# Kernel tuning notes

Measured on AMD Instinct MI355X. Metric: run time of the kernel, lower is better.

## Reference

```python
import jax, jax.numpy as jnp
import numpy as np

B, A, F, D, C = 256, 128, 512, 6, 512  # batch, max_atoms, atom_features, max_degree, conv_width


def setup_inputs() -> dict:
    key = jax.random.key(0)
    k1, k2, k3, k4 = jax.random.split(key, 4)
    atoms = jax.random.normal(k1, (B, A, F), dtype=jnp.float32)
    # neighbour indices in [0, A); pad entries beyond each atom's degree with -1
    neigh = jax.random.randint(k2, (B, A, D), 0, A)
    deg = jax.random.randint(k3, (B, A, 1), 0, D)  # degrees in 0..D-1
    bonds = jnp.where(jnp.arange(D)[None, None, :] < deg, neigh, -1)
    # one Dense(conv_width) per degree: stacked kernels [D, F, C] and biases [D, C]
    W = jax.random.normal(k4, (D, F, C), dtype=jnp.float32) * 0.02
    b = jnp.zeros((D, C), dtype=jnp.float32)
    return {"atoms": atoms, "bonds": bonds, "W": W, "b": b}


def reference(atoms, bonds, W, b):
    d_max = bonds.shape[-1]
    # per-atom degree = count of non -1 neighbour slots  [B, A, 1]
    degrees = jnp.sum(bonds != -1, axis=-1, keepdims=True)
    # shift lookup by 1 so that padded (-1) neighbours index a zero row
    padded = jnp.pad(atoms, ((0, 0), (1, 1), (0, 0)))  # [B, A+2, F]
    idx = bonds + 1  # [B, A, D]
    # per-sample gather of neighbour features -> [B, A, D, F]
    neigh_feats = jax.vmap(lambda ref, i: ref[i])(padded, idx)
    summed = jnp.sum(neigh_feats, axis=2) + atoms  # [B, A, F]
    # apply all degree-specific dense layers, then mask-select by degree
    dense = jnp.einsum('baf,dfc->badc', summed, W) + b  # [B, A, D, C]
    masks = (degrees[..., None] == jnp.arange(d_max).reshape(1, 1, d_max, 1)).astype(dense.dtype)
    return jnp.sum(dense * masks, axis=2)  # [B, A, C]
```

## Files before the change

### kernel.cpp

```cpp
#include <hip/hip_runtime.h>
#include <hip/hip_bf16.h>


#define NB 256
#define NA 128
#define NF 512
#define ND 6
#define NC 512
#define NATOMS (NB * NA)

#define NT_TRANS 1536
#define NT_BUCK  32

typedef __attribute__((ext_vector_type(8))) short frag8;
typedef __attribute__((ext_vector_type(4))) float f32x4;
typedef __attribute__((ext_vector_type(4))) unsigned int u32x4;

static __device__ inline unsigned short f2bu(float f) {
    __hip_bfloat16 h = __float2bfloat16(f);
    return *reinterpret_cast<unsigned short*>(&h);
}
static __device__ inline unsigned int pack2(float a, float b) {
    return (unsigned int)f2bu(a) | ((unsigned int)f2bu(b) << 16);
}
static __device__ inline float b2f(unsigned short u) {
    __hip_bfloat16 h;
    *reinterpret_cast<unsigned short*>(&h) = u;
    return __bfloat162float(h);
}
static __device__ inline void async16(const void* g, void* l) {
    __builtin_amdgcn_global_load_lds(
        (const __attribute__((address_space(1))) void*)g,
        (__attribute__((address_space(3))) void*)l, 16, 0, 0);
}

__global__ __launch_bounds__(256) void prep_misc(
    const float* __restrict__ W, __hip_bfloat16* __restrict__ Wt,
    const int* __restrict__ bonds, int* __restrict__ counts,
    int* __restrict__ bucket) {
    const int bid = blockIdx.x;
    const int tid = threadIdx.x;
    __shared__ float t[32][33];
    __shared__ int lcnt[ND];
    __shared__ int lbase[ND];

    if (bid < NT_TRANS) {
        const int tx = tid & 31, ty = tid >> 5;
        const int c0 = (bid & 15) * 32;
        const int f0 = ((bid >> 4) & 15) * 32;
        const int d  = bid >> 8;
        #pragma unroll
        for (int r = 0; r < 32; r += 8)
            t[ty + r][tx] =
                W[((size_t)(d * NF + f0 + ty + r)) * NC + c0 + tx];
        __syncthreads();
        #pragma unroll
        for (int r = 0; r < 32; r += 8)
            Wt[((size_t)(d * NC + c0 + ty + r)) * NF + f0 + tx] =
                __float2bfloat16(t[tx][ty + r]);
        return;
    }
    const int b = bid - NT_TRANS;
    if (tid < ND) lcnt[tid] = 0;
    __syncthreads();
    int deg[4], loc[4], gg[4];
    #pragma unroll
    for (int i = 0; i < 4; ++i) {
        int g = b * 1024 + i * 256 + tid;
        gg[i] = g;
        int dg = 0;
        #pragma unroll
        for (int j = 0; j < ND; ++j) dg += (bonds[g * ND + j] >= 0);
        deg[i] = dg;
        loc[i] = atomicAdd(&lcnt[dg], 1);
    }
    __syncthreads();
    if (tid < ND) lbase[tid] = atomicAdd(&counts[tid], lcnt[tid]);
    __syncthreads();
    #pragma unroll
    for (int i = 0; i < 4; ++i)
        bucket[deg[i] * NATOMS + lbase[deg[i]] + loc[i]] = gg[i];
}

__global__ __launch_bounds__(512, 2) void sum_mol(
    const float* __restrict__ atoms, const int* __restrict__ bonds,
    __hip_bfloat16* __restrict__ summed) {
    __shared__ __align__(16) __hip_bfloat16 mol[NA * NF];
    char* molB = (char*)mol;
    const int m   = blockIdx.x;
    const int tid = threadIdx.x;

    const float4* a4 = (const float4*)atoms + (size_t)m * (NA * NF / 4);
    #pragma unroll 4
    for (int i = 0; i < 32; ++i) {
        float4 v = a4[i * 512 + tid];
        const int r  = i * 4 + (tid >> 7);
        const int co = tid & 127;
        uint2 pk; pk.x = pack2(v.x, v.y); pk.y = pack2(v.z, v.w);
        *(uint2*)(molB + r * 1024 + (((co >> 1) ^ (r & 7)) << 4) + (co & 1) * 8) = pk;
    }
    __syncthreads();

    const int a  = tid >> 2;
    const int qd = tid & 3;
    const int* bd = bonds + (size_t)(m * NA + a) * ND;
    int   nb[ND], x7[ND];
    float msk[ND];
    #pragma unroll
    for (int j = 0; j < ND; ++j) {
        int n = bd[j];
        msk[j] = (n >= 0) ? 1.0f : 0.0f;
        nb[j]  = (n >= 0) ? n : 0;
        x7[j]  = nb[j] & 7;
    }
    const int a7 = a & 7;

    u32x4 psum[16];
    #pragma unroll
    for (int ci = 0; ci < 16; ++ci) {
        const int c = qd * 16 + ci;
        const frag8 s = *(const frag8*)(molB + a * 1024 + ((c ^ a7) << 4));
        float acc[8];
        #pragma unroll
        for (int e = 0; e < 8; ++e) acc[e] = b2f((unsigned short)s[e]);
        #pragma unroll
        for (int j = 0; j < ND; ++j) {
            const frag8 v = *(const frag8*)(molB + nb[j] * 1024 + ((c ^ x7[j]) << 4));
            #pragma unroll
            for (int e = 0; e < 8; ++e)
                acc[e] = fmaf(b2f((unsigned short)v[e]), msk[j], acc[e]);
        }
        u32x4 o;
        o[0] = pack2(acc[0], acc[1]); o[1] = pack2(acc[2], acc[3]);
        o[2] = pack2(acc[4], acc[5]); o[3] = pack2(acc[6], acc[7]);
        psum[ci] = o;
    }

    __syncthreads();
    #pragma unroll
    for (int ci = 0; ci < 16; ++ci) {
        const int c = qd * 16 + ci;
        *(u32x4*)(molB + a * 1024 + ((c ^ a7) << 4)) = psum[ci];
    }
    __syncthreads();

    const int chunk = tid & 63;
    char* dst = (char*)summed + (size_t)m * (NA * NF * 2);
    #pragma unroll
    for (int t = 0; t < 16; ++t) {
        const int row = t * 8 + (tid >> 6);
        u32x4 v = *(const u32x4*)(molB + row * 1024 + ((chunk ^ (row & 7)) << 4));
        *(u32x4*)(dst + row * 1024 + chunk * 16) = v;
    }
}

__global__ __launch_bounds__(512, 4) void gemm_deg(
    const __hip_bfloat16* __restrict__ summed, const __hip_bfloat16* __restrict__ Wt,
    const float* __restrict__ bias, const int* __restrict__ counts,
    const int* __restrict__ bucket, float* __restrict__ out) {
    const int L  = blockIdx.x + 24 * blockIdx.y;
    const int q  = L >> 3;
    const int p  = ((q >> 1) << 3) + (L & 7);
    const int d  = p % ND;
    const int m0 = (p / ND) * 128;
    const int n0 = (q & 1) * 256;
    const int Md = counts[d];
    if (m0 >= Md) return;

    __shared__ __align__(16) char smem[74240];
    char* const sAb   = smem;
    char* const sBb   = smem + 24576;
    int*  const sRows = (int*)(smem + 73728);

    const int tid = threadIdx.x;
    if (tid < 128) {
        int r = m0 + tid;
        sRows[tid] = (r < Md) ? bucket[d * NATOMS + r] : -1;
    }
    __syncthreads();

    const int lane = tid & 63;
    const int w    = tid >> 6;

    const int sr = lane >> 2;
    const int sl = lane & 3;
    const int gseg = sl ^ ((sr >> 1) & 3);

    const char* smB = (const char*)summed;
    const char* wtB = (const char*)Wt + (size_t)(d * NC + n0) * 1024;
    int g0 = sRows[w * 16 + sr];
    const size_t gA0 = (size_t)((g0 < 0) ? 0 : g0) * 1024;
    const size_t gB0 = (size_t)(w * 16 + sr) * 1024;
    const size_t gB1 = (size_t)(128 + w * 16 + sr) * 1024;

    const int quad = lane >> 4, l16 = lane & 15;
    const int xr2  = (l16 >> 1) & 3;
    const int wy = w >> 2, wx = w & 3;

    f32x4 acc[4][4];
    #pragma unroll
    for (int i = 0; i < 4; ++i)
        #pragma unroll
        for (int j = 0; j < 4; ++j) acc[i][j] = (f32x4)0.0f;

    auto stage = [&](int buf, int kt) {
        const int koff = kt * 64 + gseg * 16;
        async16(smB + gA0 + koff, sAb + buf * 8192 + w * 1024);
        async16(wtB + gB0 + koff, sBb + buf * 16384 + w * 1024);
        async16(wtB + gB1 + koff, sBb + buf * 16384 + 8192 + w * 1024);
    };
    auto compute = [&](int buf) {
        const __hip_bfloat16* A  = (const __hip_bfloat16*)(sAb + buf * 8192);
        const __hip_bfloat16* Bm = (const __hip_bfloat16*)(sBb + buf * 16384);
        frag8 aF[4], bF[4];
        #pragma unroll
        for (int i = 0; i < 4; ++i)
            aF[i] = *(const frag8*)&A[(wy * 64 + i * 16 + l16) * 32 +
                                      ((quad ^ xr2) << 3)];
        #pragma unroll
        for (int j = 0; j < 4; ++j)
            bF[j] = *(const frag8*)&Bm[(wx * 64 + j * 16 + l16) * 32 +
                                       ((quad ^ xr2) << 3)];
        #pragma unroll
        for (int i = 0; i < 4; ++i)
            #pragma unroll
            for (int j = 0; j < 4; ++j)
                acc[i][j] = __builtin_amdgcn_mfma_f32_16x16x32_bf16(
                    aF[i], bF[j], acc[i][j], 0, 0, 0);
    };

    stage(0, 0);
    stage(1, 1);
    #pragma unroll
    for (int kt = 0; kt < NF / 32; ++kt) {
        if (kt < NF / 32 - 1)
            asm volatile("s_waitcnt vmcnt(3)" ::: "memory");
        else
            asm volatile("s_waitcnt vmcnt(0)" ::: "memory");
        __builtin_amdgcn_sched_barrier(0);
        __builtin_amdgcn_s_barrier();
        if (kt + 2 < NF / 32) stage((kt + 2) % 3, kt + 2);
        __builtin_amdgcn_s_setprio(1);
        compute(kt % 3);
        __builtin_amdgcn_s_setprio(0);
    }

    const int chunk = tid & 63;
    const f32x4 bv = *(const f32x4*)&bias[d * NC + n0 + chunk * 4];
    float* cs = (float*)smem;

    #pragma unroll
    for (int s = 0; s < 2; ++s) {
        __syncthreads();
        if (wy == s) {
            #pragma unroll
            for (int i = 0; i < 4; ++i)
                #pragma unroll
                for (int j = 0; j < 4; ++j)
                    #pragma unroll
                    for (int r = 0; r < 4; ++r)
                        cs[(i * 16 + quad * 4 + r) * 256 + wx * 64 + j * 16 + l16] =
                            acc[i][j][r];
        }
        __syncthreads();
        #pragma unroll
        for (int t = 0; t < 8; ++t) {
            const int row = t * 8 + (tid >> 6);
            const int g   = sRows[s * 64 + row];
            if (g >= 0) {
                f32x4 v = *(const f32x4*)&cs[row * 256 + chunk * 4];
                v += bv;
                __builtin_nontemporal_store(
                    v, (f32x4*)(out + (size_t)g * NC + n0 + chunk * 4));
            }
        }
    }
}

extern "C" void kernel_launch(void* const* d_in, const int* in_sizes, int n_in,
                              void* d_out, int out_size, void* d_ws, size_t ws_size,
                              hipStream_t stream) {
    const float* atoms = (const float*)d_in[0];
    const int*   bonds = (const int*)d_in[1];
    const float* W     = (const float*)d_in[2];
    const float* bias  = (const float*)d_in[3];
    float* out = (float*)d_out;

    char* ws = (char*)d_ws;
    int* counts = (int*)ws;
    int* bucket = (int*)(ws + 1024);
    __hip_bfloat16* Wt     = (__hip_bfloat16*)(ws + 1024 + 786432);
    __hip_bfloat16* summed = (__hip_bfloat16*)(ws + 1024 + 786432 + 3145728);

    hipMemsetAsync(counts, 0, 1024, stream);

    prep_misc<<<NT_TRANS + NT_BUCK, 256, 0, stream>>>(W, Wt, bonds, counts, bucket);

    sum_mol<<<NB, 512, 0, stream>>>(atoms, bonds, summed);

    gemm_deg<<<dim3(24, 128), 512, 0, stream>>>(
        summed, Wt, bias, counts, bucket, out);
}
```

Baseline: 166.6 us.

## Write summed rows in degree-sorted order so GEMM A-loads are contiguous

The bucketing pass now also records an inverse map giving each atom's degree and rank. sum_mol uses it, plus a prefix over the degree counts, to scatter each summed row straight into a degree-sorted position. The GEMM then reads A rows contiguously from dBase+m0 instead of gathering through bucket indices. Atom loads also become nontemporal. The intent is better locality for the GEMM's A loads, at the cost of scattered row writes in sum_mol and an extra inverse-index array. sum_mol now depends on counts being complete when it launches.

```diff
diff --git a/kernel.cpp b/kernel.cpp
--- a/kernel.cpp
+++ b/kernel.cpp
@@ -37,7 +37,7 @@
 __global__ __launch_bounds__(256) void prep_misc(
     const float* __restrict__ W, __hip_bfloat16* __restrict__ Wt,
     const int* __restrict__ bonds, int* __restrict__ counts,
-    int* __restrict__ bucket) {
+    int* __restrict__ bucket, int* __restrict__ inv) {
     const int bid = blockIdx.x;
     const int tid = threadIdx.x;
     __shared__ float t[32][33];
@@ -78,25 +78,39 @@
     if (tid < ND) lbase[tid] = atomicAdd(&counts[tid], lcnt[tid]);
     __syncthreads();
     #pragma unroll
-    for (int i = 0; i < 4; ++i)
-        bucket[deg[i] * NATOMS + lbase[deg[i]] + loc[i]] = gg[i];
+    for (int i = 0; i < 4; ++i) {
+        const int r = lbase[deg[i]] + loc[i];
+        bucket[deg[i] * NATOMS + r] = gg[i];
+        inv[gg[i]] = (deg[i] << 16) | r;
+    }
 }
 
 __global__ __launch_bounds__(512, 2) void sum_mol(
     const float* __restrict__ atoms, const int* __restrict__ bonds,
+    const int* __restrict__ counts, const int* __restrict__ inv,
     __hip_bfloat16* __restrict__ summed) {
     __shared__ __align__(16) __hip_bfloat16 mol[NA * NF];
+    __shared__ int sdst[NA];
     char* molB = (char*)mol;
     const int m   = blockIdx.x;
     const int tid = threadIdx.x;
 
-    const float4* a4 = (const float4*)atoms + (size_t)m * (NA * NF / 4);
+    if (tid < NA) {
+        const int iv = inv[m * NA + tid];
+        const int d  = iv >> 16, r = iv & 0xffff;
+        int base = 0;
+        #pragma unroll
+        for (int k = 0; k < ND; ++k) base += (k < d) ? counts[k] : 0;
+        sdst[tid] = base + r;
+    }
+
+    const f32x4* a4 = (const f32x4*)atoms + (size_t)m * (NA * NF / 4);
     #pragma unroll 4
     for (int i = 0; i < 32; ++i) {
-        float4 v = a4[i * 512 + tid];
+        f32x4 v = __builtin_nontemporal_load(&a4[i * 512 + tid]);
         const int r  = i * 4 + (tid >> 7);
         const int co = tid & 127;
-        uint2 pk; pk.x = pack2(v.x, v.y); pk.y = pack2(v.z, v.w);
+        uint2 pk; pk.x = pack2(v[0], v[1]); pk.y = pack2(v[2], v[3]);
         *(uint2*)(molB + r * 1024 + (((co >> 1) ^ (r & 7)) << 4) + (co & 1) * 8) = pk;
     }
     __syncthreads();
@@ -145,12 +159,12 @@
     __syncthreads();
 
     const int chunk = tid & 63;
-    char* dst = (char*)summed + (size_t)m * (NA * NF * 2);
     #pragma unroll
     for (int t = 0; t < 16; ++t) {
         const int row = t * 8 + (tid >> 6);
         u32x4 v = *(const u32x4*)(molB + row * 1024 + ((chunk ^ (row & 7)) << 4));
-        *(u32x4*)(dst + row * 1024 + chunk * 16) = v;
+        char* dst = (char*)summed + (size_t)sdst[row] * 1024;
+        *(u32x4*)(dst + chunk * 16) = v;
     }
 }
 
@@ -166,6 +180,9 @@
     const int n0 = (q & 1) * 256;
     const int Md = counts[d];
     if (m0 >= Md) return;
+    int dBase = 0;
+    #pragma unroll
+    for (int k = 0; k < ND; ++k) dBase += (k < d) ? counts[k] : 0;
 
     __shared__ __align__(16) char smem[74240];
     char* const sAb   = smem;
@@ -188,8 +205,7 @@
 
     const char* smB = (const char*)summed;
     const char* wtB = (const char*)Wt + (size_t)(d * NC + n0) * 1024;
-    int g0 = sRows[w * 16 + sr];
-    const size_t gA0 = (size_t)((g0 < 0) ? 0 : g0) * 1024;
+    const size_t gA0 = (size_t)(dBase + m0 + w * 16 + sr) * 1024;
     const size_t gB0 = (size_t)(w * 16 + sr) * 1024;
     const size_t gB1 = (size_t)(128 + w * 16 + sr) * 1024;
 
@@ -289,14 +305,16 @@
     char* ws = (char*)d_ws;
     int* counts = (int*)ws;
     int* bucket = (int*)(ws + 1024);
-    __hip_bfloat16* Wt     = (__hip_bfloat16*)(ws + 1024 + 786432);
-    __hip_bfloat16* summed = (__hip_bfloat16*)(ws + 1024 + 786432 + 3145728);
-
-    hipMemsetAsync(counts, 0, 1024, stream);
-
-    prep_misc<<<NT_TRANS + NT_BUCK, 256, 0, stream>>>(W, Wt, bonds, counts, bucket);
-
-    sum_mol<<<NB, 512, 0, stream>>>(atoms, bonds, summed);
+    int* inv    = (int*)(ws + 1024 + 786432);
+    __hip_bfloat16* Wt     = (__hip_bfloat16*)(ws + 918528);
+    __hip_bfloat16* summed = (__hip_bfloat16*)(ws + 918528 + 3145728);
+
+    (void)hipMemsetAsync(counts, 0, 1024, stream);
+
+    prep_misc<<<NT_TRANS + NT_BUCK, 256, 0, stream>>>(
+        W, Wt, bonds, counts, bucket, inv);
+
+    sum_mol<<<NB, 512, 0, stream>>>(atoms, bonds, counts, inv, summed);
 
     gemm_deg<<<dim3(24, 128), 512, 0, stream>>>(
         summed, Wt, bias, counts, bucket, out);
```

Result: no change. 165.8 us (-0.5%).
